# Performance work log

Hardware: AMD Instinct MI355X
Metric: run time of the kernel (lower is better)

Reference implementation:

```python
import jax, jax.numpy as jnp
import numpy as np

VOCAB = 100000
DIM = 128
B = 16384
C_MAX = 10
K_NEG = 5


def setup_inputs() -> dict:
    key = jax.random.key(0)
    k1, k2, k3, k4, k5, k6 = jax.random.split(key, 6)
    bound = 0.5 / DIM
    return {
        "target_words": jax.random.randint(k1, (B,), 0, VOCAB),
        "context_words": jax.random.randint(k2, (B, C_MAX), 0, VOCAB),
        "context_lens": jax.random.randint(k3, (B,), 0, C_MAX + 1),
        "negative_words": jax.random.randint(k4, (B, K_NEG), 0, VOCAB),
        # input embeddings init: uniform(-0.5/dim, 0.5/dim); output init zeros in the
        # original, but we use small random values so gradients/scores are non-trivial.
        "in_emb": jax.random.uniform(k5, (VOCAB, DIM), jnp.float32, -bound, bound),
        "out_emb": jax.random.normal(k6, (VOCAB, DIM), jnp.float32) * 0.01,
    }


def reference(target_words, context_words, context_lens, negative_words, in_emb, out_emb):
    t = in_emb[target_words]                      # (B, D)
    c = out_emb[context_words]                    # (B, C, D)
    n = out_emb[negative_words]                   # (B, K, D)

    pos_scores = jnp.einsum("bd,bcd->bc", t, c)   # (B, C)
    neg_scores = jnp.einsum("bd,bkd->bk", t, n)   # (B, K)

    mask = (jnp.arange(C_MAX)[None, :] < context_lens[:, None]).astype(t.dtype)
    lens = context_lens.astype(t.dtype)
    has_ctx = lens > 0

    # per-sample mean of -logsigmoid over valid contexts; skip samples with 0 contexts
    pos_per = -jnp.sum(jax.nn.log_sigmoid(pos_scores) * mask, axis=1)
    pos_per = jnp.where(has_ctx, pos_per / jnp.maximum(lens, 1.0), 0.0)

    neg_per = -jnp.mean(jax.nn.log_sigmoid(-neg_scores), axis=1)
    neg_per = jnp.where(has_ctx, neg_per, 0.0)    # original `continue` skips negatives too

    positive_loss = jnp.sum(pos_per) / B
    negative_loss = jnp.sum(neg_per) / B
    return positive_loss, negative_loss
```

## Files before the change

kernel.cpp:

```cpp
#include <hip/hip_runtime.h>
#include <math.h>
#include <stdint.h>

#define VOCAB 100000
#define DIM   128
#define BATCH 16384
#define CMAX  10
#define KNEG  5
#define NSCORE (CMAX + KNEG)
#define JPAD  16

__device__ __forceinline__ float log_sigmoid(float x) {
    return fminf(x, 0.0f) - log1pf(expf(-fabsf(x)));
}

#define DPP_ADD_STEP(v, ctrl)                                                  \
    v += __int_as_float(__builtin_amdgcn_update_dpp(                           \
        0, __float_as_int(v), (ctrl), 0xF, 0xF, false))

__device__ __forceinline__ float dpp_reduce32_to_lane31(float v) {
    DPP_ADD_STEP(v, 0x111);
    DPP_ADD_STEP(v, 0x112);
    DPP_ADD_STEP(v, 0x114);
    DPP_ADD_STEP(v, 0x118);
    DPP_ADD_STEP(v, 0x142);
    return v;
}

__global__ __launch_bounds__(256) void score_kernel(
    const int*   __restrict__ tgt,
    const int*   __restrict__ ctx,
    const int*   __restrict__ neg,
    const float* __restrict__ in_emb,
    const float* __restrict__ out_emb,
    float*       __restrict__ scores,
    float*       __restrict__ out)
{
    const int tid  = threadIdx.x;
    const int sub  = tid & 31;
    const int unit = (blockIdx.x * 256 + tid) >> 5;
    const int b    = unit >> 4;
    const int j    = unit & 15;

    if (blockIdx.x == 0 && tid < 2) out[tid] = 0.0f;

    int word;
    if (j < CMAX)        word = ctx[b * CMAX + j];
    else if (j < NSCORE) word = neg[b * KNEG + (j - CMAX)];
    else                 word = 0;
    const int t_word = tgt[b];

    const float4 tv = ((const float4*)(in_emb  + (size_t)t_word * DIM))[sub];
    const float4 rv = ((const float4*)(out_emb + (size_t)word   * DIM))[sub];

    float p = tv.x * rv.x + tv.y * rv.y + tv.z * rv.z + tv.w * rv.w;

    p = dpp_reduce32_to_lane31(p);

    if (sub == 31) scores[unit] = p;
}

__global__ __launch_bounds__(256) void loss_kernel(
    const float* __restrict__ scores,
    const int*   __restrict__ lens,
    float*       __restrict__ out)
{
    const int tid = threadIdx.x;
    const int b   = blockIdx.x * 256 + tid;

    const int len = lens[b];
    const float* s = scores + (size_t)b * JPAD;

    float sc[NSCORE];
#pragma unroll
    for (int j = 0; j < NSCORE; ++j) sc[j] = s[j];

    float pos_acc = 0.0f;
#pragma unroll
    for (int c = 0; c < CMAX; ++c)
        if (c < len) pos_acc += log_sigmoid(sc[c]);
    float neg_acc = 0.0f;
#pragma unroll
    for (int k = 0; k < KNEG; ++k)
        neg_acc += log_sigmoid(-sc[CMAX + k]);

    float pos_per = 0.0f, neg_per = 0.0f;
    if (len > 0) {
        pos_per = -pos_acc / (float)len;
        neg_per = -neg_acc * (1.0f / KNEG);
    }

#pragma unroll
    for (int m = 32; m >= 1; m >>= 1) {
        pos_per += __shfl_xor(pos_per, m, 64);
        neg_per += __shfl_xor(neg_per, m, 64);
    }
    __shared__ float s_pos[4];
    __shared__ float s_neg[4];
    const int wave = tid >> 6;
    if ((tid & 63) == 0) { s_pos[wave] = pos_per; s_neg[wave] = neg_per; }
    __syncthreads();
    if (tid == 0) {
        float ps = s_pos[0] + s_pos[1] + s_pos[2] + s_pos[3];
        float ns = s_neg[0] + s_neg[1] + s_neg[2] + s_neg[3];
        atomicAdd(&out[0], ps * (1.0f / BATCH));
        atomicAdd(&out[1], ns * (1.0f / BATCH));
    }
}

extern "C" void kernel_launch(void* const* d_in, const int* in_sizes, int n_in,
                              void* d_out, int out_size, void* d_ws, size_t ws_size,
                              hipStream_t stream) {
    const int*   tgt     = (const int*)  d_in[0];
    const int*   ctx     = (const int*)  d_in[1];
    const int*   lens    = (const int*)  d_in[2];
    const int*   neg     = (const int*)  d_in[3];
    const float* in_emb  = (const float*)d_in[4];
    const float* out_emb = (const float*)d_in[5];
    float* out    = (float*)d_out;
    float* scores = (float*)d_ws;

    score_kernel<<<(BATCH * JPAD) / 8, 256, 0, stream>>>(
        tgt, ctx, neg, in_emb, out_emb, scores, out);

    loss_kernel<<<BATCH / 256, 256, 0, stream>>>(scores, lens, out);
}
```

Measured before the change: 150.1 us.

## Compute four scores per half-wave, reusing target row with inline-asm loads

Each 32-lane group now computes four scores instead of one, so it loads the target embedding row once and reuses it across four context or negative rows. This cuts redundant target-row loads and the grid size by four. The loads use inline global_load_dwordx4 with 32-bit offsets and an explicit waitcnt, keeping all five loads in flight together. In exchange each thread uses more registers and there are fewer waves to hide latency, and the asm bypasses compiler scheduling.

Result: faster. 136.0 us (-9.4%).

```diff
diff --git a/kernel.cpp b/kernel.cpp
--- a/kernel.cpp
+++ b/kernel.cpp
@@ -9,6 +9,8 @@
 #define KNEG  5
 #define NSCORE (CMAX + KNEG)
 #define JPAD  16
+
+typedef float f32x4 __attribute__((ext_vector_type(4)));
 
 __device__ __forceinline__ float log_sigmoid(float x) {
     return fminf(x, 0.0f) - log1pf(expf(-fabsf(x)));
@@ -38,26 +40,56 @@
 {
     const int tid  = threadIdx.x;
     const int sub  = tid & 31;
-    const int unit = (blockIdx.x * 256 + tid) >> 5;
-    const int b    = unit >> 4;
-    const int j    = unit & 15;
+    const int task = (blockIdx.x * 256 + tid) >> 5;
+    const int b    = task >> 2;
+    const int g    = task & 3;
+    const int j0   = g * 4;
 
     if (blockIdx.x == 0 && tid < 2) out[tid] = 0.0f;
 
-    int word;
-    if (j < CMAX)        word = ctx[b * CMAX + j];
-    else if (j < NSCORE) word = neg[b * KNEG + (j - CMAX)];
-    else                 word = 0;
     const int t_word = tgt[b];
+    int words[4];
+#pragma unroll
+    for (int jj = 0; jj < 4; ++jj) {
+        const int j = j0 + jj;
+        if (j < CMAX)        words[jj] = ctx[b * CMAX + j];
+        else if (j < NSCORE) words[jj] = neg[b * KNEG + (j - CMAX)];
+        else                 words[jj] = 0;
+    }
 
-    const float4 tv = ((const float4*)(in_emb  + (size_t)t_word * DIM))[sub];
-    const float4 rv = ((const float4*)(out_emb + (size_t)word   * DIM))[sub];
+    const uint32_t sub16 = (uint32_t)sub * 16u;
 
-    float p = tv.x * rv.x + tv.y * rv.y + tv.z * rv.z + tv.w * rv.w;
+    f32x4 tv;
+    {
+        uint32_t off = (uint32_t)t_word * (DIM * 4u) + sub16;
+        asm volatile("global_load_dwordx4 %0, %1, %2"
+                     : "=v"(tv) : "v"(off), "s"(in_emb));
+    }
+    f32x4 rv[4];
+#pragma unroll
+    for (int jj = 0; jj < 4; ++jj) {
+        uint32_t off = (uint32_t)words[jj] * (DIM * 4u) + sub16;
+        asm volatile("global_load_dwordx4 %0, %1, %2"
+                     : "=v"(rv[jj]) : "v"(off), "s"(out_emb));
+    }
+    asm volatile("s_waitcnt vmcnt(0)"
+                 : "+v"(tv), "+v"(rv[0]), "+v"(rv[1]), "+v"(rv[2]), "+v"(rv[3])
+                 :
+                 : "memory");
 
-    p = dpp_reduce32_to_lane31(p);
+    float p[4];
+#pragma unroll
+    for (int jj = 0; jj < 4; ++jj) {
+        float d = tv.x * rv[jj].x + tv.y * rv[jj].y +
+                  tv.z * rv[jj].z + tv.w * rv[jj].w;
+        p[jj] = dpp_reduce32_to_lane31(d);
+    }
 
-    if (sub == 31) scores[unit] = p;
+    if (sub == 31) {
+        float* s = scores + (size_t)b * JPAD + j0;
+#pragma unroll
+        for (int jj = 0; jj < 4; ++jj) s[jj] = p[jj];
+    }
 }
 
 __global__ __launch_bounds__(256) void loss_kernel(
@@ -120,7 +152,7 @@
     float* out    = (float*)d_out;
     float* scores = (float*)d_ws;
 
-    score_kernel<<<(BATCH * JPAD) / 8, 256, 0, stream>>>(
+    score_kernel<<<(BATCH * 4) / 8, 256, 0, stream>>>(
         tgt, ctx, neg, in_emb, out_emb, scores, out);
 
     loss_kernel<<<BATCH / 256, 256, 0, stream>>>(scores, lens, out);
```
